# Kernel optimization log

Measured on AMD Instinct MI355X. Metric: run time of the kernel, lower is better.

The kernel has to match this reference:

```python
import jax, jax.numpy as jnp
import numpy as np

B, T, N, D, F, ORDER = 16, 12, 1024, 64, 64, 2
EPS = 1e-5  # BatchNorm eps (eval mode, running stats)


def setup_inputs() -> dict:
    key = jax.random.key(0)
    ks = jax.random.split(key, 8)
    C_eff = (ORDER + 1) * D  # (order*support_len + 1) * c_in = 192
    return {
        "x": jax.random.normal(ks[0], (B, T, N, D), jnp.float32),
        "A": jax.random.uniform(ks[1], (B, N, N), jnp.float32),  # dynamic per-sample adjacency
        "conv_w": jax.random.normal(ks[2], (F, C_eff), jnp.float32) / np.float32(np.sqrt(C_eff)),
        "conv_b": jnp.zeros((F,), jnp.float32),
        "bn_gamma": jnp.ones((F,), jnp.float32),
        "bn_beta": jnp.zeros((F,), jnp.float32),
        "bn_mean": 0.1 * jax.random.normal(ks[3], (F,), jnp.float32),
        "bn_var": jax.random.uniform(ks[4], (F,), jnp.float32) + 0.5,
        "gru_ff_w": jax.random.normal(ks[5], (T, 2 * F, 2 * F), jnp.float32) / np.float32(np.sqrt(2 * F)),
        "gru_ff_b": jnp.zeros((T, 2 * F), jnp.float32),
        "gru_zff_w": jax.random.normal(ks[6], (T, 2 * F, F), jnp.float32) / np.float32(np.sqrt(2 * F)),
        "gru_zff_b": jnp.zeros((T, F), jnp.float32),
    }


def _forward(x, A, conv_w, conv_b, bn_gamma, bn_beta, bn_mean, bn_var,
             gru_ff_w, gru_ff_b, gru_zff_w, gru_zff_b):
    # ---- DiffusionGraphEncoder ----
    xt = jnp.transpose(x, (0, 3, 2, 1))  # (B, C, N, T), matches torch transpose(1,3)
    outs = [xt]
    cur = xt
    for _ in range(ORDER):  # nconv: einsum('ncvl,nwv->ncwl')
        cur = jnp.einsum('bcvt,bwv->bcwt', cur, A)
        outs.append(cur)
    h = jnp.concatenate(outs, axis=1)        # (B, 3C, N, T)
    h = jnp.transpose(h, (0, 3, 2, 1))       # (B, T, N, C_eff)
    # ---- MLP1x1: 1x1 conv + eval-mode BatchNorm + relu ----
    y = jnp.einsum('btnc,fc->btnf', h, conv_w) + conv_b
    y = (y - bn_mean) * jax.lax.rsqrt(bn_var + EPS) * bn_gamma + bn_beta
    y = jax.nn.relu(y)  # dropout is identity at inference
    # ---- GRUEncoder: distinct GRUCellLite per timestep ----
    xs = jnp.transpose(y, (1, 0, 2, 3))      # (T, B, N, F)
    h0 = jnp.zeros((B, N, F), y.dtype)

    def step(hprev, inp):
        xt_, wff, bff, wzff, bzff = inp
        ru = jax.nn.sigmoid(jnp.concatenate([xt_, hprev], -1) @ wff + bff)
        r, u = ru[..., :F], ru[..., F:]
        z = jnp.tanh(jnp.concatenate([xt_, r * hprev], -1) @ wzff + bzff)
        hn = u * z + (1.0 - u) * hprev
        return hn, hn

    _, hs = jax.lax.scan(step, h0, (xs, gru_ff_w, gru_ff_b, gru_zff_w, gru_zff_b))
    return jnp.transpose(hs, (1, 0, 2, 3))   # (B, T, N, F)


def reference(x, A, conv_w, conv_b, bn_gamma, bn_beta, bn_mean, bn_var,
              gru_ff_w, gru_ff_b, gru_zff_w, gru_zff_b):
    return _forward(x, A, conv_w, conv_b, bn_gamma, bn_beta, bn_mean, bn_var,
                    gru_ff_w, gru_ff_b, gru_zff_w, gru_zff_b)
```

## Files before the change

### kernel.cpp

```cpp
#include <hip/hip_runtime.h>
#include <cstdint>
#include <cstddef>

#define NB 16
#define TT 12
#define NN 1024
#define DD 64
#define FF 64
#define JT 768

typedef __attribute__((ext_vector_type(8))) short v8s;
typedef __attribute__((ext_vector_type(4))) short v4s;
typedef __attribute__((ext_vector_type(4))) float v4f;

__device__ __forceinline__ float sigmoidf_(float v) { return 1.0f / (1.0f + expf(-v)); }

__device__ __forceinline__ float bf2f(unsigned short h) {
    union { unsigned int u; float f; } x; x.u = ((unsigned int)h) << 16; return x.f;
}
__device__ __forceinline__ unsigned short f2bf(float f) {
    union { float f; unsigned int u; } x; x.f = f;
    return (unsigned short)((x.u + 0x7fffu + ((x.u >> 16) & 1u)) >> 16);
}

__device__ __forceinline__ void gload16(const void* g, void* lds) {
    __builtin_amdgcn_global_load_lds(
        (const __attribute__((address_space(1))) void*)g,
        (__attribute__((address_space(3))) void*)lds, 16, 0, 0);
}

__global__ __launch_bounds__(256) void split_A(
    const float* __restrict__ A, unsigned short* __restrict__ Ah,
    unsigned short* __restrict__ Al)
{
    const size_t i0 = ((size_t)blockIdx.x * 256 + threadIdx.x) * 16;
    float v[16];
#pragma unroll
    for (int s = 0; s < 4; ++s)
        *(float4*)&v[s * 4] = *(const float4*)&A[i0 + s * 4];
    v8s h0, h1, l0, l1;
#pragma unroll
    for (int q = 0; q < 8; ++q) {
        unsigned short h = f2bf(v[q]);
        h0[q] = (short)h; l0[q] = (short)f2bf(v[q] - bf2f(h));
    }
#pragma unroll
    for (int q = 0; q < 8; ++q) {
        unsigned short h = f2bf(v[8 + q]);
        h1[q] = (short)h; l1[q] = (short)f2bf(v[8 + q] - bf2f(h));
    }
    *(v8s*)&Ah[i0] = h0; *(v8s*)&Ah[i0 + 8] = h1;
    *(v8s*)&Al[i0] = l0; *(v8s*)&Al[i0 + 8] = l1;
}

__global__ __launch_bounds__(256) void xsplitT(
    const float* __restrict__ x, unsigned short* __restrict__ Th,
    unsigned short* __restrict__ Tl)
{
    __shared__ float tile[64][68];
    const int v0 = blockIdx.x * 64, t = blockIdx.y, b = blockIdx.z;
    const int tid = threadIdx.x;
    {
        const int r = tid >> 2, q = (tid & 3) * 16;
#pragma unroll
        for (int s = 0; s < 4; ++s) {
            const float4 w = *(const float4*)&x[(((size_t)b * TT + t) * NN + v0 + r) * DD + q + s * 4];
            tile[r][q + s * 4 + 0] = w.x; tile[r][q + s * 4 + 1] = w.y;
            tile[r][q + s * 4 + 2] = w.z; tile[r][q + s * 4 + 3] = w.w;
        }
    }
    __syncthreads();
    {
        const int d = tid >> 2, vc = (tid & 3) * 16;
        const size_t base = ((size_t)b * JT + t * 64 + d) * 1024 + v0 + vc;
        v8s h0, h1, l0, l1;
#pragma unroll
        for (int s = 0; s < 8; ++s) {
            const float f = tile[vc + s][d];
            unsigned short h = f2bf(f);
            h0[s] = (short)h; l0[s] = (short)f2bf(f - bf2f(h));
        }
#pragma unroll
        for (int s = 0; s < 8; ++s) {
            const float f = tile[vc + 8 + s][d];
            unsigned short h = f2bf(f);
            h1[s] = (short)h; l1[s] = (short)f2bf(f - bf2f(h));
        }
        *(v8s*)&Th[base] = h0; *(v8s*)&Th[base + 8] = h1;
        *(v8s*)&Tl[base] = l0; *(v8s*)&Tl[base + 8] = l1;
    }
}

template<bool PAIROUT>
__global__ __launch_bounds__(256, 2) void gemm_bf(
    const unsigned short* __restrict__ Ah, const unsigned short* __restrict__ Al,
    const unsigned short* __restrict__ Bh, const unsigned short* __restrict__ Bl,
    unsigned short* __restrict__ Ch, unsigned short* __restrict__ Cl,
    float* __restrict__ Cf)
{
    __shared__ unsigned short LA[2][2][4096];
    __shared__ unsigned short LB[2][2][4096];

    const int wg = blockIdx.x;
    const int nlin = (wg & 7) * 96 + (wg >> 3);
    const int b  = nlin / 48;
    const int rr = nlin % 48;
    const int m0 = (rr / 6) * 128, n0 = (rr % 6) * 128;

    const int tid = threadIdx.x, lane = tid & 63, wid = tid >> 6;
    const int lr = lane & 15, hi = lane >> 4;
    const int wr = wid >> 1, wc = wid & 1;

    auto stage = [&](int buf, int kt) {
        const int rA = lane >> 2, kc = (lane & 3) * 8;
#pragma unroll
        for (int p = 0; p < 2; ++p) {
            const int c = wid * 2 + p;
            const size_t ga = ((size_t)b * 1024 + m0 + c * 16 + rA) * 1024 + kt * 32 + kc;
            gload16(Ah + ga, &LA[buf][0][c * 512]);
            gload16(Al + ga, &LA[buf][1][c * 512]);
            const size_t gb = ((size_t)b * JT + n0 + c * 16 + rA) * 1024 + kt * 32 + kc;
            gload16(Bh + gb, &LB[buf][0][c * 512]);
            gload16(Bl + gb, &LB[buf][1][c * 512]);
        }
    };

    v4f acc[4][4];
#pragma unroll
    for (int i = 0; i < 4; ++i)
#pragma unroll
        for (int j = 0; j < 4; ++j) acc[i][j] = (v4f){0.f, 0.f, 0.f, 0.f};

    stage(0, 0);
    __syncthreads();
    int cur = 0;
    for (int kt = 0; kt < 32; ++kt) {
        if (kt + 1 < 32) stage(cur ^ 1, kt + 1);
        v8s ah[4], al[4], bh[4], bl[4];
#pragma unroll
        for (int f = 0; f < 4; ++f) {
            const int m = wr * 64 + f * 16 + lr;
            ah[f] = *(const v8s*)&LA[cur][0][m * 32 + hi * 8];
            al[f] = *(const v8s*)&LA[cur][1][m * 32 + hi * 8];
        }
#pragma unroll
        for (int f = 0; f < 4; ++f) {
            const int n = wc * 64 + f * 16 + lr;
            bh[f] = *(const v8s*)&LB[cur][0][n * 32 + hi * 8];
            bl[f] = *(const v8s*)&LB[cur][1][n * 32 + hi * 8];
        }
#pragma unroll
        for (int fi = 0; fi < 4; ++fi)
#pragma unroll
            for (int fj = 0; fj < 4; ++fj) {
                acc[fi][fj] = __builtin_amdgcn_mfma_f32_16x16x32_bf16(ah[fi], bh[fj], acc[fi][fj], 0, 0, 0);
                acc[fi][fj] = __builtin_amdgcn_mfma_f32_16x16x32_bf16(ah[fi], bl[fj], acc[fi][fj], 0, 0, 0);
                acc[fi][fj] = __builtin_amdgcn_mfma_f32_16x16x32_bf16(al[fi], bh[fj], acc[fi][fj], 0, 0, 0);
                acc[fi][fj] = __builtin_amdgcn_mfma_f32_16x16x32_bf16(al[fi], bl[fj], acc[fi][fj], 0, 0, 0);
            }
        __syncthreads();
        cur ^= 1;
    }

#pragma unroll
    for (int fi = 0; fi < 4; ++fi)
#pragma unroll
        for (int fj = 0; fj < 4; ++fj) {
            const int n  = n0 + wc * 64 + fj * 16 + lr;
            const int mb = m0 + wr * 64 + fi * 16 + hi * 4;
            const size_t o = ((size_t)b * JT + n) * 1024 + mb;
            if (PAIROUT) {
                v4s vh, vl;
#pragma unroll
                for (int r = 0; r < 4; ++r) {
                    const float v = acc[fi][fj][r];
                    const unsigned short h = f2bf(v);
                    vh[r] = (short)h; vl[r] = (short)f2bf(v - bf2f(h));
                }
                *(v4s*)&Ch[o] = vh;
                *(v4s*)&Cl[o] = vl;
            } else {
                float4 v = {acc[fi][fj][0], acc[fi][fj][1], acc[fi][fj][2], acc[fi][fj][3]};
                *(float4*)&Cf[o] = v;
            }
        }
}

template<bool XFROMX>
__global__ __launch_bounds__(256, 4) void gemm_f32(
    const float* __restrict__ Aop, const float* __restrict__ Xin,
    float* __restrict__ Xout)
{
    __shared__ float As[2][16 * 132];
    __shared__ float Bs[2][16 * 128];
    const int wg  = blockIdx.x;
    const int nlin = (wg & 7) * 96 + (wg >> 3);
    const int b  = nlin / 48;
    const int rr = nlin % 48;
    const int rb = rr / 6, cb = rr % 6;
    const int w0 = rb * 128, j0 = cb * 128;
    const int tid = threadIdx.x;
    const int rg = tid >> 4, cg = tid & 15;
    const int row0 = rg * 8;

    auto stage = [&](int buf, int kt) {
        const float* Ab = Aop + (size_t)b * NN * NN;
#pragma unroll
        for (int p = 0; p < 2; ++p) {
            const int c  = tid + p * 256;
            const int w  = c >> 2;
            const int k4 = (c & 3) * 4;
            const float4 v = *(const float4*)&Ab[(size_t)(w0 + w) * NN + kt * 16 + k4];
            As[buf][(k4 + 0) * 132 + w] = v.x;
            As[buf][(k4 + 1) * 132 + w] = v.y;
            As[buf][(k4 + 2) * 132 + w] = v.z;
            As[buf][(k4 + 3) * 132 + w] = v.w;
        }
#pragma unroll
        for (int p = 0; p < 2; ++p) {
            const int c = tid + p * 256;
            const int k = c >> 5;
            const int j = (c & 31) * 4;
            float4 v;
            if (XFROMX) {
                const int t = cb * 2 + (j >> 6);
                const int d = j & 63;
                v = *(const float4*)&Xin[(((size_t)b * TT + t) * NN + (size_t)kt * 16 + k) * DD + d];
            } else {
                v = *(const float4*)&Xin[((size_t)b * NN + (size_t)kt * 16 + k) * JT + j0 + j];
            }
            *(float4*)&Bs[buf][k * 128 + j] = v;
        }
    };

    float acc[8][8];
#pragma unroll
    for (int i = 0; i < 8; ++i)
#pragma unroll
        for (int j = 0; j < 8; ++j) acc[i][j] = 0.0f;

    stage(0, 0);
    __syncthreads();
    int cur = 0;
    for (int kt = 0; kt < 64; ++kt) {
        if (kt + 1 < 64) stage(cur ^ 1, kt + 1);
#pragma unroll
        for (int k = 0; k < 16; ++k) {
            float a[8], bb[8];
            *(float4*)&a[0]  = *(const float4*)&As[cur][k * 132 + row0];
            *(float4*)&a[4]  = *(const float4*)&As[cur][k * 132 + row0 + 4];
            *(float4*)&bb[0] = *(const float4*)&Bs[cur][k * 128 + cg * 4];
            *(float4*)&bb[4] = *(const float4*)&Bs[cur][k * 128 + 64 + cg * 4];
#pragma unroll
            for (int i = 0; i < 8; ++i)
#pragma unroll
                for (int j = 0; j < 8; ++j)
                    acc[i][j] = fmaf(a[i], bb[j], acc[i][j]);
        }
        __syncthreads();
        cur ^= 1;
    }
#pragma unroll
    for (int i = 0; i < 8; ++i) {
        float4 v0 = {acc[i][0], acc[i][1], acc[i][2], acc[i][3]};
        float4 v1 = {acc[i][4], acc[i][5], acc[i][6], acc[i][7]};
        float* dst = Xout + ((size_t)b * NN + w0 + row0 + i) * JT + j0;
        *(float4*)&dst[cg * 4]      = v0;
        *(float4*)&dst[64 + cg * 4] = v1;
    }
}

template<bool PAIRS>
__global__ __launch_bounds__(256) void conv_bn_relu(
    const float* __restrict__ x,
    const unsigned short* __restrict__ X1h, const unsigned short* __restrict__ X1l,
    const float* __restrict__ X2T,
    const float* __restrict__ X1f, const float* __restrict__ X2f,
    const float* __restrict__ W,
    const float* __restrict__ convb, const float* __restrict__ gamma,
    const float* __restrict__ beta,  const float* __restrict__ mean,
    const float* __restrict__ var,   float* __restrict__ y)
{
    __shared__ float As[64][132];
    __shared__ float Ws[64][68];
    const int nb = blockIdx.x, t = blockIdx.y, b = blockIdx.z;
    const int n0 = nb * 128;
    const int tid = threadIdx.x;
    const int rg = tid >> 4, cg = tid & 15;
    const int row0 = rg * 8, f0 = cg * 4;

    float acc[8][4];
#pragma unroll
    for (int i = 0; i < 8; ++i)
#pragma unroll
        for (int j = 0; j < 4; ++j) acc[i][j] = 0.0f;

    for (int kt = 0; kt < 3; ++kt) {
        __syncthreads();
        if (kt == 0) {
            const float* src = x + (((size_t)b * TT + t) * NN + n0) * DD;
#pragma unroll
            for (int p = 0; p < 8; ++p) {
                const int row = (tid >> 4) + p * 16;
                const int c4  = (tid & 15) * 4;
                const float4 v = *(const float4*)&src[(size_t)row * DD + c4];
                As[c4 + 0][row] = v.x; As[c4 + 1][row] = v.y;
                As[c4 + 2][row] = v.z; As[c4 + 3][row] = v.w;
            }
        } else if (PAIRS) {
            if (kt == 1) {
#pragma unroll
                for (int p = 0; p < 4; ++p) {
                    const int pos = p * 256 + tid;
                    const int c = pos >> 4, rw = (pos & 15) * 8;
                    const size_t o = ((size_t)b * JT + t * 64 + c) * 1024 + n0 + rw;
                    const v8s hv = *(const v8s*)&X1h[o];
                    const v8s lv = *(const v8s*)&X1l[o];
#pragma unroll
                    for (int q = 0; q < 8; ++q)
                        As[c][rw + q] = bf2f((unsigned short)hv[q]) + bf2f((unsigned short)lv[q]);
                }
            } else {
#pragma unroll
                for (int p = 0; p < 8; ++p) {
                    const int pos = p * 256 + tid;
                    const int c = pos >> 5, rw = (pos & 31) * 4;
                    const float4 v = *(const float4*)&X2T[((size_t)b * JT + t * 64 + c) * 1024 + n0 + rw];
                    As[c][rw + 0] = v.x; As[c][rw + 1] = v.y;
                    As[c][rw + 2] = v.z; As[c][rw + 3] = v.w;
                }
            }
        } else {
            const float* src = ((kt == 1) ? X1f : X2f) + ((size_t)b * NN + n0) * JT + t * DD;
#pragma unroll
            for (int p = 0; p < 8; ++p) {
                const int row = (tid >> 4) + p * 16;
                const int c4  = (tid & 15) * 4;
                const float4 v = *(const float4*)&src[(size_t)row * JT + c4];
                As[c4 + 0][row] = v.x; As[c4 + 1][row] = v.y;
                As[c4 + 2][row] = v.z; As[c4 + 3][row] = v.w;
            }
        }
#pragma unroll
        for (int p = 0; p < 4; ++p) {
            const int f  = (tid >> 4) + p * 16;
            const int c4 = (tid & 15) * 4;
            const float4 v = *(const float4*)&W[f * 192 + kt * 64 + c4];
            Ws[c4 + 0][f] = v.x; Ws[c4 + 1][f] = v.y;
            Ws[c4 + 2][f] = v.z; Ws[c4 + 3][f] = v.w;
        }
        __syncthreads();
#pragma unroll
        for (int k = 0; k < 64; ++k) {
            float a[8], w[4];
            *(float4*)&a[0] = *(const float4*)&As[k][row0];
            *(float4*)&a[4] = *(const float4*)&As[k][row0 + 4];
            *(float4*)&w[0] = *(const float4*)&Ws[k][f0];
#pragma unroll
            for (int i = 0; i < 8; ++i)
#pragma unroll
                for (int j = 0; j < 4; ++j)
                    acc[i][j] = fmaf(a[i], w[j], acc[i][j]);
        }
    }
    float s[4], off[4];
#pragma unroll
    for (int j = 0; j < 4; ++j) {
        const int f = f0 + j;
        const float sc = gamma[f] / sqrtf(var[f] + 1e-5f);
        s[j]   = sc;
        off[j] = (convb[f] - mean[f]) * sc + beta[f];
    }
#pragma unroll
    for (int i = 0; i < 8; ++i) {
        float4 v;
        v.x = fmaxf(acc[i][0] * s[0] + off[0], 0.0f);
        v.y = fmaxf(acc[i][1] * s[1] + off[1], 0.0f);
        v.z = fmaxf(acc[i][2] * s[2] + off[2], 0.0f);
        v.w = fmaxf(acc[i][3] * s[3] + off[3], 0.0f);
        *(float4*)&y[(((size_t)b * TT + t) * NN + n0 + row0 + i) * FF + f0] = v;
    }
}

__global__ __launch_bounds__(256) void wprep3(
    const float* __restrict__ wff, const float* __restrict__ wzff,
    unsigned short* __restrict__ WF, unsigned short* __restrict__ WZ)
{
    const int t = blockIdx.x;
    unsigned short* F = WF + (size_t)t * 40960;
    for (int e = threadIdx.x; e < 8192; e += 256) {
        const int o = e >> 6, k = e & 63;
        const float vx = wff[((size_t)t * 128 + k) * 128 + o];
        const unsigned short xh = f2bf(vx);
        const float r1 = vx - bf2f(xh);
        const unsigned short xm = f2bf(r1);
        const unsigned short xl = f2bf(r1 - bf2f(xm));
        F[0 * 8192 + o * 64 + k] = xh;
        F[1 * 8192 + o * 64 + k] = xm;
        F[2 * 8192 + o * 64 + k] = xl;
        const float vh = wff[((size_t)t * 128 + 64 + k) * 128 + o];
        const unsigned short hh = f2bf(vh);
        const unsigned short hl = f2bf(vh - bf2f(hh));
        F[3 * 8192 + o * 64 + k] = hh;
        F[4 * 8192 + o * 64 + k] = hl;
    }
    unsigned short* Z = WZ + (size_t)t * 20480;
    for (int e = threadIdx.x; e < 4096; e += 256) {
        const int o = e >> 6, k = e & 63;
        const float vx = wzff[((size_t)t * 128 + k) * 64 + o];
        const unsigned short xh = f2bf(vx);
        const float r1 = vx - bf2f(xh);
        const unsigned short xm = f2bf(r1);
        const unsigned short xl = f2bf(r1 - bf2f(xm));
        Z[0 * 4096 + o * 64 + k] = xh;
        Z[1 * 4096 + o * 64 + k] = xm;
        Z[2 * 4096 + o * 64 + k] = xl;
        const float vr = wzff[((size_t)t * 128 + 64 + k) * 64 + o];
        const unsigned short rh = f2bf(vr);
        const unsigned short rl = f2bf(vr - bf2f(rh));
        Z[3 * 4096 + o * 64 + k] = rh;
        Z[4 * 4096 + o * 64 + k] = rl;
    }
}

__global__ __launch_bounds__(256, 2) void gru5(
    const float* __restrict__ y,
    const unsigned short* __restrict__ WF, const unsigned short* __restrict__ WZ,
    const float* __restrict__ bff, const float* __restrict__ bzff,
    float* __restrict__ out)
{
    __shared__ unsigned short Ahp[4096];
    __shared__ unsigned short Rhp[4096];
    __shared__ float Hs[32][68];

    const int tid = threadIdx.x, lane = tid & 63, w = tid >> 6;
    const int lr = lane & 15, hi = lane >> 4;
    const int b = blockIdx.x >> 5, n0 = (blockIdx.x & 31) * 32;

    for (int i = tid; i < 4096; i += 256) { Ahp[i] = 0; Rhp[i] = 0; }
    for (int i = tid; i < 32 * 68; i += 256) (&Hs[0][0])[i] = 0.0f;
    __syncthreads();

    auto loadx = [&](int t, v8s xa[2][2][3]) {
        const float* yb = y + (((size_t)b * TT + t) * NN + n0) * 64;
#pragma unroll
        for (int mf = 0; mf < 2; ++mf)
#pragma unroll
            for (int kc = 0; kc < 2; ++kc) {
                const int m = mf * 16 + lr;
                float xv[8];
                *(float4*)&xv[0] = *(const float4*)&yb[m * 64 + kc * 32 + hi * 8];
                *(float4*)&xv[4] = *(const float4*)&yb[m * 64 + kc * 32 + hi * 8 + 4];
                v8s h3, m3, l3;
#pragma unroll
                for (int q = 0; q < 8; ++q) {
                    const float v = xv[q];
                    const unsigned short hh = f2bf(v);
                    const float r1 = v - bf2f(hh);
                    const unsigned short mm = f2bf(r1);
                    const unsigned short ll = f2bf(r1 - bf2f(mm));
                    h3[q] = (short)hh; m3[q] = (short)mm; l3[q] = (short)ll;
                }
                xa[mf][kc][0] = h3; xa[mf][kc][1] = m3; xa[mf][kc][2] = l3;
            }
    };
    auto xru_mfma = [&](int t, const v8s xa[2][2][3], v4f xacc[2][2]) {
#pragma unroll
        for (int of = 0; of < 2; ++of) {
            const int o = (2 * w + of) * 16 + lr;
            v8s wx[2][3];
#pragma unroll
            for (int kc = 0; kc < 2; ++kc)
#pragma unroll
                for (int lev = 0; lev < 3; ++lev)
                    wx[kc][lev] = *(const v8s*)&WF[((size_t)t * 5 + lev) * 8192 + o * 64 + kc * 32 + hi * 8];
#pragma unroll
            for (int mf = 0; mf < 2; ++mf)
#pragma unroll
                for (int kc = 0; kc < 2; ++kc) {
                    v4f a = xacc[of][mf];
                    a = __builtin_amdgcn_mfma_f32_16x16x32_bf16(xa[mf][kc][0], wx[kc][0], a, 0, 0, 0);
                    a = __builtin_amdgcn_mfma_f32_16x16x32_bf16(xa[mf][kc][0], wx[kc][1], a, 0, 0, 0);
                    a = __builtin_amdgcn_mfma_f32_16x16x32_bf16(xa[mf][kc][1], wx[kc][0], a, 0, 0, 0);
                    a = __builtin_amdgcn_mfma_f32_16x16x32_bf16(xa[mf][kc][0], wx[kc][2], a, 0, 0, 0);
                    a = __builtin_amdgcn_mfma_f32_16x16x32_bf16(xa[mf][kc][1], wx[kc][1], a, 0, 0, 0);
                    a = __builtin_amdgcn_mfma_f32_16x16x32_bf16(xa[mf][kc][2], wx[kc][0], a, 0, 0, 0);
                    xacc[of][mf] = a;
                }
        }
    };
    auto xz_mfma = [&](int t, const v8s xa[2][2][3], v4f xacc[2][2]) {
#pragma unroll
        for (int of = 0; of < 2; ++of) {
            const int o = (w & 1) * 32 + of * 16 + lr;
            v8s wx[2][3];
#pragma unroll
            for (int kc = 0; kc < 2; ++kc)
#pragma unroll
                for (int lev = 0; lev < 3; ++lev)
                    wx[kc][lev] = *(const v8s*)&WZ[((size_t)t * 5 + lev) * 4096 + o * 64 + kc * 32 + hi * 8];
#pragma unroll
            for (int mf = 0; mf < 2; ++mf)
#pragma unroll
                for (int kc = 0; kc < 2; ++kc) {
                    v4f a = xacc[of][mf];
                    a = __builtin_amdgcn_mfma_f32_16x16x32_bf16(xa[mf][kc][0], wx[kc][0], a, 0, 0, 0);
                    a = __builtin_amdgcn_mfma_f32_16x16x32_bf16(xa[mf][kc][0], wx[kc][1], a, 0, 0, 0);
                    a = __builtin_amdgcn_mfma_f32_16x16x32_bf16(xa[mf][kc][1], wx[kc][0], a, 0, 0, 0);
                    a = __builtin_amdgcn_mfma_f32_16x16x32_bf16(xa[mf][kc][0], wx[kc][2], a, 0, 0, 0);
                    a = __builtin_amdgcn_mfma_f32_16x16x32_bf16(xa[mf][kc][1], wx[kc][1], a, 0, 0, 0);
                    a = __builtin_amdgcn_mfma_f32_16x16x32_bf16(xa[mf][kc][2], wx[kc][0], a, 0, 0, 0);
                    xacc[of][mf] = a;
                }
        }
    };

    v4f xru[2][2], xz[2][2];
#pragma unroll
    for (int of = 0; of < 2; ++of)
#pragma unroll
        for (int mf = 0; mf < 2; ++mf) {
            xru[of][mf] = (v4f){0.f, 0.f, 0.f, 0.f};
            xz[of][mf]  = (v4f){0.f, 0.f, 0.f, 0.f};
        }
    {
        v8s xa0[2][2][3];
        loadx(0, xa0);
        xru_mfma(0, xa0, xru);
        xz_mfma(0, xa0, xz);
    }

    for (int t = 0; t < TT; ++t) {
        const int hasNext = (t + 1 < TT);
        v8s ha[2][2][2];
#pragma unroll
        for (int mf = 0; mf < 2; ++mf)
#pragma unroll
            for (int kc = 0; kc < 2; ++kc) {
                const int m = mf * 16 + lr;
                const int base = m * 128 + kc * 32 + hi * 8;
                const int sw = (m & 7) << 3;
                ha[mf][kc][0] = *(const v8s*)&Ahp[base ^ sw];
                ha[mf][kc][1] = *(const v8s*)&Ahp[(base + 64) ^ sw];
            }
        __syncthreads();

        v4f acc[2][2];
#pragma unroll
        for (int of = 0; of < 2; ++of)
#pragma unroll
            for (int mf = 0; mf < 2; ++mf) acc[of][mf] = xru[of][mf];

        v8s xan[2][2][3];
        v4f xruN[2][2], xzN[2][2];
#pragma unroll
        for (int of = 0; of < 2; ++of)
#pragma unroll
            for (int mf = 0; mf < 2; ++mf) {
                xruN[of][mf] = (v4f){0.f, 0.f, 0.f, 0.f};
                xzN[of][mf]  = (v4f){0.f, 0.f, 0.f, 0.f};
            }
        if (hasNext) loadx(t + 1, xan);

        {
#pragma unroll
            for (int of = 0; of < 2; ++of) {
                const int o = (2 * w + of) * 16 + lr;
                v8s wh_[2][2];
#pragma unroll
                for (int kc = 0; kc < 2; ++kc)
#pragma unroll
                    for (int lev = 0; lev < 2; ++lev)
                        wh_[kc][lev] = *(const v8s*)&WF[((size_t)t * 5 + 3 + lev) * 8192 + o * 64 + kc * 32 + hi * 8];
#pragma unroll
                for (int mf = 0; mf < 2; ++mf)
#pragma unroll
                    for (int kc = 0; kc < 2; ++kc) {
                        v4f a = acc[of][mf];
                        a = __builtin_amdgcn_mfma_f32_16x16x32_bf16(ha[mf][kc][0], wh_[kc][0], a, 0, 0, 0);
                        a = __builtin_amdgcn_mfma_f32_16x16x32_bf16(ha[mf][kc][0], wh_[kc][1], a, 0, 0, 0);
                        a = __builtin_amdgcn_mfma_f32_16x16x32_bf16(ha[mf][kc][1], wh_[kc][0], a, 0, 0, 0);
                        acc[of][mf] = a;
                    }
            }
            if (hasNext) xru_mfma(t + 1, xan, xruN);
        }
        __syncthreads();

        float u_[2][2][4];
#pragma unroll
        for (int of = 0; of < 2; ++of) {
            const int o = (2 * w + of) * 16 + lr;
            const float bv = bff[(size_t)t * 128 + o];
#pragma unroll
            for (int mf = 0; mf < 2; ++mf)
#pragma unroll
                for (int q = 0; q < 4; ++q) {
                    const float g = sigmoidf_(acc[of][mf][q] + bv);
                    if (w < 2) {
                        const int m = mf * 16 + hi * 4 + q;
                        const float rh = g * Hs[m][o];
                        const unsigned short h = f2bf(rh);
                        const unsigned short l = f2bf(rh - bf2f(h));
                        const int sw = (m & 7) << 3;
                        Rhp[(m * 128 + o) ^ sw]      = h;
                        Rhp[(m * 128 + 64 + o) ^ sw] = l;
                    } else {
                        u_[of][mf][q] = g;
                    }
                }
        }
        __syncthreads();

        v8s ra[2][2][2];
#pragma unroll
        for (int mf = 0; mf < 2; ++mf)
#pragma unroll
            for (int kc = 0; kc < 2; ++kc) {
                const int m = mf * 16 + lr;
                const int base = m * 128 + kc * 32 + hi * 8;
                const int sw = (m & 7) << 3;
                ra[mf][kc][0] = *(const v8s*)&Rhp[base ^ sw];
                ra[mf][kc][1] = *(const v8s*)&Rhp[(base + 64) ^ sw];
            }
        __syncthreads();

        v4f accz[2][2];
#pragma unroll
        for (int of = 0; of < 2; ++of)
#pragma unroll
            for (int mf = 0; mf < 2; ++mf) accz[of][mf] = xz[of][mf];

        {
#pragma unroll
            for (int of = 0; of < 2; ++of) {
                const int o = (w & 1) * 32 + of * 16 + lr;
                v8s wr_[2][2];
#pragma unroll
                for (int kc = 0; kc < 2; ++kc)
#pragma unroll
                    for (int lev = 0; lev < 2; ++lev)
                        wr_[kc][lev] = *(const v8s*)&WZ[((size_t)t * 5 + 3 + lev) * 4096 + o * 64 + kc * 32 + hi * 8];
#pragma unroll
                for (int mf = 0; mf < 2; ++mf)
#pragma unroll
                    for (int kc = 0; kc < 2; ++kc) {
                        v4f a = accz[of][mf];
                        a = __builtin_amdgcn_mfma_f32_16x16x32_bf16(ra[mf][kc][0], wr_[kc][0], a, 0, 0, 0);
                        a = __builtin_amdgcn_mfma_f32_16x16x32_bf16(ra[mf][kc][0], wr_[kc][1], a, 0, 0, 0);
                        a = __builtin_amdgcn_mfma_f32_16x16x32_bf16(ra[mf][kc][1], wr_[kc][0], a, 0, 0, 0);
                        accz[of][mf] = a;
                    }
            }
            if (hasNext) xz_mfma(t + 1, xan, xzN);
        }
        __syncthreads();

        if (w >= 2) {
#pragma unroll
            for (int of = 0; of < 2; ++of) {
                const int o = (w & 1) * 32 + of * 16 + lr;
                const float bz = bzff[(size_t)t * 64 + o];
#pragma unroll
                for (int mf = 0; mf < 2; ++mf)
#pragma unroll
                    for (int q = 0; q < 4; ++q) {
                        const int m = mf * 16 + hi * 4 + q;
                        const float z = tanhf(accz[of][mf][q] + bz);
                        const float u = u_[of][mf][q];
                        const float hn = u * z + (1.0f - u) * Hs[m][o];
                        Hs[m][o] = hn;
                        const unsigned short h = f2bf(hn);
                        const unsigned short l = f2bf(hn - bf2f(h));
                        const int sw = (m & 7) << 3;
                        Ahp[(m * 128 + o) ^ sw]      = h;
                        Ahp[(m * 128 + 64 + o) ^ sw] = l;
                        out[(((size_t)b * TT + t) * NN + n0 + m) * 64 + o] = hn;
                    }
            }
        }
        __syncthreads();

#pragma unroll
        for (int of = 0; of < 2; ++of)
#pragma unroll
            for (int mf = 0; mf < 2; ++mf) {
                xru[of][mf] = xruN[of][mf];
                xz[of][mf]  = xzN[of][mf];
            }
    }
}

__global__ __launch_bounds__(256) void gru_all(
    const float* __restrict__ y,    const float* __restrict__ wff,
    const float* __restrict__ bff,  const float* __restrict__ wzff,
    const float* __restrict__ bzff, float* __restrict__ out)
{
    __shared__ float Xs[64][36];
    __shared__ float Hs[64][36];
    __shared__ float Rs[64][36];
    __shared__ float Us[64][36];
    __shared__ float Ws[64][132];
    const int tid = threadIdx.x;
    const int mb  = blockIdx.x;
    const int b = mb >> 5, n0 = (mb & 31) * 32;
    const int rg = tid >> 5;
    const int og = tid & 31;

    for (int i = tid; i < 64 * 36; i += 256) (&Hs[0][0])[i] = 0.0f;

    for (int t = 0; t < TT; ++t) {
        {
            const float* xt = y + (((size_t)b * TT + t) * NN + n0) * DD;
            const int m = tid >> 3, c0 = (tid & 7) * 8;
            const float4 v0 = *(const float4*)&xt[m * DD + c0];
            const float4 v1 = *(const float4*)&xt[m * DD + c0 + 4];
            Xs[c0 + 0][m] = v0.x; Xs[c0 + 1][m] = v0.y;
            Xs[c0 + 2][m] = v0.z; Xs[c0 + 3][m] = v0.w;
            Xs[c0 + 4][m] = v1.x; Xs[c0 + 5][m] = v1.y;
            Xs[c0 + 6][m] = v1.z; Xs[c0 + 7][m] = v1.w;
        }
        float acc[4][4];
#pragma unroll
        for (int i = 0; i < 4; ++i)
#pragma unroll
            for (int j = 0; j < 4; ++j) acc[i][j] = 0.0f;

#pragma unroll
        for (int half = 0; half < 2; ++half) {
            __syncthreads();
#pragma unroll
            for (int p = 0; p < 8; ++p) {
                const int kk = (tid >> 5) + p * 8;
                const int o4 = (tid & 31) * 4;
                *(float4*)&Ws[kk][o4] =
                    *(const float4*)&wff[((size_t)t * 128 + half * 64 + kk) * 128 + o4];
            }
            __syncthreads();
            const float (*Asrc)[36] = half ? Hs : Xs;
#pragma unroll 4
            for (int kk = 0; kk < 64; ++kk) {
                const float4 av = *(const float4*)&Asrc[kk][rg * 4];
                const float4 wv = *(const float4*)&Ws[kk][og * 4];
                const float a0 = av.x, a1 = av.y, a2 = av.z, a3 = av.w;
                acc[0][0] = fmaf(a0, wv.x, acc[0][0]); acc[0][1] = fmaf(a0, wv.y, acc[0][1]);
                acc[0][2] = fmaf(a0, wv.z, acc[0][2]); acc[0][3] = fmaf(a0, wv.w, acc[0][3]);
                acc[1][0] = fmaf(a1, wv.x, acc[1][0]); acc[1][1] = fmaf(a1, wv.y, acc[1][1]);
                acc[1][2] = fmaf(a1, wv.z, acc[1][2]); acc[1][3] = fmaf(a1, wv.w, acc[1][3]);
                acc[2][0] = fmaf(a2, wv.x, acc[2][0]); acc[2][1] = fmaf(a2, wv.y, acc[2][1]);
                acc[2][2] = fmaf(a2, wv.z, acc[2][2]); acc[2][3] = fmaf(a2, wv.w, acc[2][3]);
                acc[3][0] = fmaf(a3, wv.x, acc[3][0]); acc[3][1] = fmaf(a3, wv.y, acc[3][1]);
                acc[3][2] = fmaf(a3, wv.z, acc[3][2]); acc[3][3] = fmaf(a3, wv.w, acc[3][3]);
            }
        }
        {
            const float4 bb4 = *(const float4*)&bff[(size_t)t * 128 + og * 4];
            float g[4][4];
#pragma unroll
            for (int i = 0; i < 4; ++i) {
                g[i][0] = sigmoidf_(acc[i][0] + bb4.x);
                g[i][1] = sigmoidf_(acc[i][1] + bb4.y);
                g[i][2] = sigmoidf_(acc[i][2] + bb4.z);
                g[i][3] = sigmoidf_(acc[i][3] + bb4.w);
            }
            if (og < 16) {
#pragma unroll
                for (int i = 0; i < 4; ++i)
#pragma unroll
                    for (int j = 0; j < 4; ++j) {
                        const int f = og * 4 + j, m = rg * 4 + i;
                        Rs[f][m] = g[i][j] * Hs[f][m];
                    }
            } else {
#pragma unroll
                for (int i = 0; i < 4; ++i)
#pragma unroll
                    for (int j = 0; j < 4; ++j)
                        Us[og * 4 + j - 64][rg * 4 + i] = g[i][j];
            }
        }
        float accz[4][2];
#pragma unroll
        for (int i = 0; i < 4; ++i) { accz[i][0] = 0.0f; accz[i][1] = 0.0f; }

#pragma unroll
        for (int half = 0; half < 2; ++half) {
            __syncthreads();
#pragma unroll
            for (int p = 0; p < 4; ++p) {
                const int kk = (tid >> 4) + p * 16;
                const int f4 = (tid & 15) * 4;
                *(float4*)&Ws[kk][f4] =
                    *(const float4*)&wzff[((size_t)t * 128 + half * 64 + kk) * 64 + f4];
            }
            __syncthreads();
            const float (*Asrc)[36] = half ? Rs : Xs;
#pragma unroll 4
            for (int kk = 0; kk < 64; ++kk) {
                const float4 av = *(const float4*)&Asrc[kk][rg * 4];
                const float2 wv = *(const float2*)&Ws[kk][og * 2];
                accz[0][0] = fmaf(av.x, wv.x, accz[0][0]); accz[0][1] = fmaf(av.x, wv.y, accz[0][1]);
                accz[1][0] = fmaf(av.y, wv.x, accz[1][0]); accz[1][1] = fmaf(av.y, wv.y, accz[1][1]);
                accz[2][0] = fmaf(av.z, wv.x, accz[2][0]); accz[2][1] = fmaf(av.z, wv.y, accz[2][1]);
                accz[3][0] = fmaf(av.w, wv.x, accz[3][0]); accz[3][1] = fmaf(av.w, wv.y, accz[3][1]);
            }
        }
        {
            const float2 bz = *(const float2*)&bzff[(size_t)t * 64 + og * 2];
            const int f0_ = og * 2;
#pragma unroll
            for (int i = 0; i < 4; ++i) {
                const int m = rg * 4 + i;
                const float z0 = tanhf(accz[i][0] + bz.x);
                const float z1 = tanhf(accz[i][1] + bz.y);
                const float u0 = Us[f0_][m],     u1 = Us[f0_ + 1][m];
                const float h0 = Hs[f0_][m],     h1 = Hs[f0_ + 1][m];
                const float hn0 = u0 * z0 + (1.0f - u0) * h0;
                const float hn1 = u1 * z1 + (1.0f - u1) * h1;
                Hs[f0_][m] = hn0; Hs[f0_ + 1][m] = hn1;
                *(float2*)&out[(((size_t)b * TT + t) * NN + n0 + m) * FF + f0_] =
                    make_float2(hn0, hn1);
            }
        }
        __syncthreads();
    }
}

extern "C" void kernel_launch(void* const* d_in, const int* in_sizes, int n_in,
                              void* d_out, int out_size, void* d_ws, size_t ws_size,
                              hipStream_t stream)
{
    const float* x        = (const float*)d_in[0];
    const float* A        = (const float*)d_in[1];
    const float* conv_w   = (const float*)d_in[2];
    const float* conv_b   = (const float*)d_in[3];
    const float* bn_gamma = (const float*)d_in[4];
    const float* bn_beta  = (const float*)d_in[5];
    const float* bn_mean  = (const float*)d_in[6];
    const float* bn_var   = (const float*)d_in[7];
    const float* gru_ff_w  = (const float*)d_in[8];
    const float* gru_ff_b  = (const float*)d_in[9];
    const float* gru_zff_w = (const float*)d_in[10];
    const float* gru_zff_b = (const float*)d_in[11];
    float* out = (float*)d_out;
    char* w = (char*)d_ws;

    const size_t szA_bf  = (size_t)NB * NN * NN * 2;
    const size_t szXT_bf = (size_t)NB * JT * NN * 2;
    const size_t needFast = 2 * szA_bf + 2 * szXT_bf + 2 * szXT_bf;

    dim3 gconv(8, TT, NB);

    if (ws_size >= needFast) {
        unsigned short* Ah2 = (unsigned short*)(w);
        unsigned short* Al2 = (unsigned short*)(w + szA_bf);
        unsigned short* X1h = (unsigned short*)(w + 2 * szA_bf);
        unsigned short* X1l = (unsigned short*)(w + 2 * szA_bf + szXT_bf);
        char* slot = w + 2 * szA_bf + 2 * szXT_bf;
        unsigned short* xh = (unsigned short*)slot;
        unsigned short* xl = (unsigned short*)(slot + szXT_bf);
        float* X2T = (float*)slot;
        float* yb = (float*)w;
        unsigned short* WF = (unsigned short*)(w + 50331648);
        unsigned short* WZ = (unsigned short*)(w + 50331648 + 983040);

        xsplitT<<<dim3(16, TT, NB), 256, 0, stream>>>(x, xh, xl);
        split_A<<<4096, 256, 0, stream>>>(A, Ah2, Al2);
        gemm_bf<true ><<<768, 256, 0, stream>>>(Ah2, Al2, xh,  xl,  X1h, X1l, nullptr);
        gemm_bf<false><<<768, 256, 0, stream>>>(Ah2, Al2, X1h, X1l, nullptr, nullptr, X2T);
        conv_bn_relu<true><<<gconv, 256, 0, stream>>>(x, X1h, X1l, X2T, nullptr, nullptr,
                                                      conv_w, conv_b, bn_gamma, bn_beta,
                                                      bn_mean, bn_var, yb);
        wprep3<<<TT, 256, 0, stream>>>(gru_ff_w, gru_zff_w, WF, WZ);
        gru5<<<512, 256, 0, stream>>>(yb, WF, WZ, gru_ff_b, gru_zff_b, out);
    } else {
        const size_t szX = (size_t)NB * NN * JT;
        float* X1 = (float*)w;
        float* X2 = X1 + szX;
        float* yb = X2 + szX;
        gemm_f32<true ><<<768, 256, 0, stream>>>(A, x,  X1);
        gemm_f32<false><<<768, 256, 0, stream>>>(A, X1, X2);
        conv_bn_relu<false><<<gconv, 256, 0, stream>>>(x, nullptr, nullptr, nullptr, X1, X2,
                                                       conv_w, conv_b, bn_gamma, bn_beta,
                                                       bn_mean, bn_var, yb);
        gru_all<<<512, 256, 0, stream>>>(yb, gru_ff_w, gru_ff_b,
                                         gru_zff_w, gru_zff_b, out);
    }
}
```

Baseline: 512.9 us.

## Widen GEMM tiles to 128x192, drop GRU barriers, use fast sigmoid/tanh

The bf16-split GEMM tile grows from 128x128 to 128x192 so each workgroup reuses its A tile across more columns, and the grid drops from 768 to 512 blocks. This costs more accumulator registers and LDS, which may lower occupancy. In the GRU kernel, two __syncthreads per stage are removed, and sigmoid/tanh switch to __expf/__fdividef approximations. Removing those barriers may introduce LDS races between the reads of Ahp/Rhp and the later writes to them.

```diff
diff --git a/kernel.cpp b/kernel.cpp
--- a/kernel.cpp
+++ b/kernel.cpp
@@ -14,6 +14,14 @@
 typedef __attribute__((ext_vector_type(4))) float v4f;
 
 __device__ __forceinline__ float sigmoidf_(float v) { return 1.0f / (1.0f + expf(-v)); }
+__device__ __forceinline__ float fsig(float v) {
+    return __fdividef(1.0f, 1.0f + __expf(-v));
+}
+__device__ __forceinline__ float ftanh(float v) {
+    v = fminf(fmaxf(v, -15.0f), 15.0f);
+    const float e = __expf(2.0f * v);
+    return __fdividef(e - 1.0f, e + 1.0f);
+}
 
 __device__ __forceinline__ float bf2f(unsigned short h) {
     union { unsigned int u; float f; } x; x.u = ((unsigned int)h) << 16; return x.f;
@@ -99,13 +107,13 @@
     float* __restrict__ Cf)
 {
     __shared__ unsigned short LA[2][2][4096];
-    __shared__ unsigned short LB[2][2][4096];
+    __shared__ unsigned short LB[2][2][6144];
 
     const int wg = blockIdx.x;
-    const int nlin = (wg & 7) * 96 + (wg >> 3);
-    const int b  = nlin / 48;
-    const int rr = nlin % 48;
-    const int m0 = (rr / 6) * 128, n0 = (rr % 6) * 128;
+    const int nlin = (wg & 7) * 64 + (wg >> 3);
+    const int b  = nlin >> 5;
+    const int rr = nlin & 31;
+    const int m0 = (rr >> 2) * 128, n0 = (rr & 3) * 192;
 
     const int tid = threadIdx.x, lane = tid & 63, wid = tid >> 6;
     const int lr = lane & 15, hi = lane >> 4;
@@ -119,24 +127,28 @@
             const size_t ga = ((size_t)b * 1024 + m0 + c * 16 + rA) * 1024 + kt * 32 + kc;
             gload16(Ah + ga, &LA[buf][0][c * 512]);
             gload16(Al + ga, &LA[buf][1][c * 512]);
+        }
+#pragma unroll
+        for (int p = 0; p < 3; ++p) {
+            const int c = wid * 3 + p;
             const size_t gb = ((size_t)b * JT + n0 + c * 16 + rA) * 1024 + kt * 32 + kc;
             gload16(Bh + gb, &LB[buf][0][c * 512]);
             gload16(Bl + gb, &LB[buf][1][c * 512]);
         }
     };
 
-    v4f acc[4][4];
+    v4f acc[4][6];
 #pragma unroll
     for (int i = 0; i < 4; ++i)
 #pragma unroll
-        for (int j = 0; j < 4; ++j) acc[i][j] = (v4f){0.f, 0.f, 0.f, 0.f};
+        for (int j = 0; j < 6; ++j) acc[i][j] = (v4f){0.f, 0.f, 0.f, 0.f};
 
     stage(0, 0);
     __syncthreads();
     int cur = 0;
     for (int kt = 0; kt < 32; ++kt) {
         if (kt + 1 < 32) stage(cur ^ 1, kt + 1);
-        v8s ah[4], al[4], bh[4], bl[4];
+        v8s ah[4], al[4], bh[6], bl[6];
 #pragma unroll
         for (int f = 0; f < 4; ++f) {
             const int m = wr * 64 + f * 16 + lr;
@@ -144,15 +156,15 @@
             al[f] = *(const v8s*)&LA[cur][1][m * 32 + hi * 8];
         }
 #pragma unroll
-        for (int f = 0; f < 4; ++f) {
-            const int n = wc * 64 + f * 16 + lr;
+        for (int f = 0; f < 6; ++f) {
+            const int n = wc * 96 + f * 16 + lr;
             bh[f] = *(const v8s*)&LB[cur][0][n * 32 + hi * 8];
             bl[f] = *(const v8s*)&LB[cur][1][n * 32 + hi * 8];
         }
 #pragma unroll
         for (int fi = 0; fi < 4; ++fi)
 #pragma unroll
-            for (int fj = 0; fj < 4; ++fj) {
+            for (int fj = 0; fj < 6; ++fj) {
                 acc[fi][fj] = __builtin_amdgcn_mfma_f32_16x16x32_bf16(ah[fi], bh[fj], acc[fi][fj], 0, 0, 0);
                 acc[fi][fj] = __builtin_amdgcn_mfma_f32_16x16x32_bf16(ah[fi], bl[fj], acc[fi][fj], 0, 0, 0);
                 acc[fi][fj] = __builtin_amdgcn_mfma_f32_16x16x32_bf16(al[fi], bh[fj], acc[fi][fj], 0, 0, 0);
@@ -165,8 +177,8 @@
 #pragma unroll
     for (int fi = 0; fi < 4; ++fi)
 #pragma unroll
-        for (int fj = 0; fj < 4; ++fj) {
-            const int n  = n0 + wc * 64 + fj * 16 + lr;
+        for (int fj = 0; fj < 6; ++fj) {
+            const int n  = n0 + wc * 96 + fj * 16 + lr;
             const int mb = m0 + wr * 64 + fi * 16 + hi * 4;
             const size_t o = ((size_t)b * JT + n) * 1024 + mb;
             if (PAIROUT) {
@@ -423,7 +435,7 @@
     }
 }
 
-__global__ __launch_bounds__(256, 2) void gru5(
+__global__ __launch_bounds__(256, 2) void gru7(
     const float* __restrict__ y,
     const unsigned short* __restrict__ WF, const unsigned short* __restrict__ WZ,
     const float* __restrict__ bff, const float* __restrict__ bzff,
@@ -543,7 +555,6 @@
                 ha[mf][kc][0] = *(const v8s*)&Ahp[base ^ sw];
                 ha[mf][kc][1] = *(const v8s*)&Ahp[(base + 64) ^ sw];
             }
-        __syncthreads();
 
         v4f acc[2][2];
 #pragma unroll
@@ -562,30 +573,27 @@
             }
         if (hasNext) loadx(t + 1, xan);
 
-        {
-#pragma unroll
-            for (int of = 0; of < 2; ++of) {
-                const int o = (2 * w + of) * 16 + lr;
-                v8s wh_[2][2];
-#pragma unroll
-                for (int kc = 0; kc < 2; ++kc)
-#pragma unroll
-                    for (int lev = 0; lev < 2; ++lev)
-                        wh_[kc][lev] = *(const v8s*)&WF[((size_t)t * 5 + 3 + lev) * 8192 + o * 64 + kc * 32 + hi * 8];
-#pragma unroll
-                for (int mf = 0; mf < 2; ++mf)
-#pragma unroll
-                    for (int kc = 0; kc < 2; ++kc) {
-                        v4f a = acc[of][mf];
-                        a = __builtin_amdgcn_mfma_f32_16x16x32_bf16(ha[mf][kc][0], wh_[kc][0], a, 0, 0, 0);
-                        a = __builtin_amdgcn_mfma_f32_16x16x32_bf16(ha[mf][kc][0], wh_[kc][1], a, 0, 0, 0);
-                        a = __builtin_amdgcn_mfma_f32_16x16x32_bf16(ha[mf][kc][1], wh_[kc][0], a, 0, 0, 0);
-                        acc[of][mf] = a;
-                    }
-            }
-            if (hasNext) xru_mfma(t + 1, xan, xruN);
-        }
-        __syncthreads();
+#pragma unroll
+        for (int of = 0; of < 2; ++of) {
+            const int o = (2 * w + of) * 16 + lr;
+            v8s wh_[2][2];
+#pragma unroll
+            for (int kc = 0; kc < 2; ++kc)
+#pragma unroll
+                for (int lev = 0; lev < 2; ++lev)
+                    wh_[kc][lev] = *(const v8s*)&WF[((size_t)t * 5 + 3 + lev) * 8192 + o * 64 + kc * 32 + hi * 8];
+#pragma unroll
+            for (int mf = 0; mf < 2; ++mf)
+#pragma unroll
+                for (int kc = 0; kc < 2; ++kc) {
+                    v4f a = acc[of][mf];
+                    a = __builtin_amdgcn_mfma_f32_16x16x32_bf16(ha[mf][kc][0], wh_[kc][0], a, 0, 0, 0);
+                    a = __builtin_amdgcn_mfma_f32_16x16x32_bf16(ha[mf][kc][0], wh_[kc][1], a, 0, 0, 0);
+                    a = __builtin_amdgcn_mfma_f32_16x16x32_bf16(ha[mf][kc][1], wh_[kc][0], a, 0, 0, 0);
+                    acc[of][mf] = a;
+                }
+        }
+        if (hasNext) xru_mfma(t + 1, xan, xruN);
 
         float u_[2][2][4];
 #pragma unroll
@@ -596,7 +604,7 @@
             for (int mf = 0; mf < 2; ++mf)
 #pragma unroll
                 for (int q = 0; q < 4; ++q) {
-                    const float g = sigmoidf_(acc[of][mf][q] + bv);
+                    const float g = fsig(acc[of][mf][q] + bv);
                     if (w < 2) {
                         const int m = mf * 16 + hi * 4 + q;
                         const float rh = g * Hs[m][o];
@@ -623,7 +631,6 @@
                 ra[mf][kc][0] = *(const v8s*)&Rhp[base ^ sw];
                 ra[mf][kc][1] = *(const v8s*)&Rhp[(base + 64) ^ sw];
             }
-        __syncthreads();
 
         v4f accz[2][2];
 #pragma unroll
@@ -631,30 +638,27 @@
 #pragma unroll
             for (int mf = 0; mf < 2; ++mf) accz[of][mf] = xz[of][mf];
 
-        {
-#pragma unroll
-            for (int of = 0; of < 2; ++of) {
-                const int o = (w & 1) * 32 + of * 16 + lr;
-                v8s wr_[2][2];
-#pragma unroll
-                for (int kc = 0; kc < 2; ++kc)
-#pragma unroll
-                    for (int lev = 0; lev < 2; ++lev)
-                        wr_[kc][lev] = *(const v8s*)&WZ[((size_t)t * 5 + 3 + lev) * 4096 + o * 64 + kc * 32 + hi * 8];
-#pragma unroll
-                for (int mf = 0; mf < 2; ++mf)
-#pragma unroll
-                    for (int kc = 0; kc < 2; ++kc) {
-                        v4f a = accz[of][mf];
-                        a = __builtin_amdgcn_mfma_f32_16x16x32_bf16(ra[mf][kc][0], wr_[kc][0], a, 0, 0, 0);
-                        a = __builtin_amdgcn_mfma_f32_16x16x32_bf16(ra[mf][kc][0], wr_[kc][1], a, 0, 0, 0);
-                        a = __builtin_amdgcn_mfma_f32_16x16x32_bf16(ra[mf][kc][1], wr_[kc][0], a, 0, 0, 0);
-                        accz[of][mf] = a;
-                    }
-            }
-            if (hasNext) xz_mfma(t + 1, xan, xzN);
-        }
-        __syncthreads();
+#pragma unroll
+        for (int of = 0; of < 2; ++of) {
+            const int o = (w & 1) * 32 + of * 16 + lr;
+            v8s wr_[2][2];
+#pragma unroll
+            for (int kc = 0; kc < 2; ++kc)
+#pragma unroll
+                for (int lev = 0; lev < 2; ++lev)
+                    wr_[kc][lev] = *(const v8s*)&WZ[((size_t)t * 5 + 3 + lev) * 4096 + o * 64 + kc * 32 + hi * 8];
+#pragma unroll
+            for (int mf = 0; mf < 2; ++mf)
+#pragma unroll
+                for (int kc = 0; kc < 2; ++kc) {
+                    v4f a = accz[of][mf];
+                    a = __builtin_amdgcn_mfma_f32_16x16x32_bf16(ra[mf][kc][0], wr_[kc][0], a, 0, 0, 0);
+                    a = __builtin_amdgcn_mfma_f32_16x16x32_bf16(ra[mf][kc][0], wr_[kc][1], a, 0, 0, 0);
+                    a = __builtin_amdgcn_mfma_f32_16x16x32_bf16(ra[mf][kc][1], wr_[kc][0], a, 0, 0, 0);
+                    accz[of][mf] = a;
+                }
+        }
+        if (hasNext) xz_mfma(t + 1, xan, xzN);
 
         if (w >= 2) {
 #pragma unroll
@@ -666,7 +670,7 @@
 #pragma unroll
                     for (int q = 0; q < 4; ++q) {
                         const int m = mf * 16 + hi * 4 + q;
-                        const float z = tanhf(accz[of][mf][q] + bz);
+                        const float z = ftanh(accz[of][mf][q] + bz);
                         const float u = u_[of][mf][q];
                         const float hn = u * z + (1.0f - u) * Hs[m][o];
                         Hs[m][o] = hn;
@@ -866,13 +870,13 @@
 
         xsplitT<<<dim3(16, TT, NB), 256, 0, stream>>>(x, xh, xl);
         split_A<<<4096, 256, 0, stream>>>(A, Ah2, Al2);
-        gemm_bf<true ><<<768, 256, 0, stream>>>(Ah2, Al2, xh,  xl,  X1h, X1l, nullptr);
-        gemm_bf<false><<<768, 256, 0, stream>>>(Ah2, Al2, X1h, X1l, nullptr, nullptr, X2T);
+        gemm_bf<true ><<<512, 256, 0, stream>>>(Ah2, Al2, xh,  xl,  X1h, X1l, nullptr);
+        gemm_bf<false><<<512, 256, 0, stream>>>(Ah2, Al2, X1h, X1l, nullptr, nullptr, X2T);
         conv_bn_relu<true><<<gconv, 256, 0, stream>>>(x, X1h, X1l, X2T, nullptr, nullptr,
                                                       conv_w, conv_b, bn_gamma, bn_beta,
                                                       bn_mean, bn_var, yb);
         wprep3<<<TT, 256, 0, stream>>>(gru_ff_w, gru_zff_w, WF, WZ);
-        gru5<<<512, 256, 0, stream>>>(yb, WF, WZ, gru_ff_b, gru_zff_b, out);
+        gru7<<<512, 256, 0, stream>>>(yb, WF, WZ, gru_ff_b, gru_zff_b, out);
     } else {
         const size_t szX = (size_t)NB * NN * JT;
         float* X1 = (float*)w;
```

After: 466.6 us. 9.0% less time.
